# Kernel optimization log

Measured on AMD Instinct MI355X. Metric: run time of the kernel, lower is better.

## Reference

```python
import jax, jax.numpy as jnp
import numpy as np

B, S, HID, NH, DH = 2, 1024, 4096, 32, 128
ACT_BITS, W_BITS = 8, 4
NEG_INF = float(np.finfo(np.float32).min)


def _qdq(x, bits):
    """Symmetric fake-quant over the last axis (per-token / per-out-channel), with STE."""
    qmax = 2.0 ** (bits - 1) - 1
    s = jnp.maximum(jnp.max(jnp.abs(x), axis=-1, keepdims=True) / qmax, 1e-8)
    q = jnp.clip(jnp.round(x / s), -qmax - 1, qmax) * s
    return x + jax.lax.stop_gradient(q - x)


def _rope_tables(seq_len, dim):
    inv_freq = 1.0 / (10000.0 ** (np.arange(0, dim, 2, dtype=np.float32) / dim))
    t = np.arange(seq_len, dtype=np.float32)
    freqs = np.outer(t, inv_freq)              # [S, DH/2]
    emb = np.concatenate([freqs, freqs], -1)   # [S, DH]
    return jnp.asarray(np.cos(emb)), jnp.asarray(np.sin(emb))


def _rotate_half(x):
    h = x.shape[-1] // 2
    return jnp.concatenate([-x[..., h:], x[..., :h]], axis=-1)


def _norm(x):
    return jnp.linalg.norm(x, axis=-1, keepdims=True)


def setup_inputs() -> dict:
    key = jax.random.key(0)
    ks = jax.random.split(key, 5)
    causal = jnp.where(jnp.tril(jnp.ones((S, S), dtype=bool)), 0.0, NEG_INF).astype(jnp.float32)
    return {
        "hidden_states": jax.random.normal(ks[0], (B, S, HID), jnp.float32),
        "wq": jax.random.normal(ks[1], (HID, HID), jnp.float32) * 0.02,
        "wk": jax.random.normal(ks[2], (HID, HID), jnp.float32) * 0.02,
        "wv": jax.random.normal(ks[3], (HID, HID), jnp.float32) * 0.02,
        "wo": jax.random.normal(ks[4], (HID, HID), jnp.float32) * 0.02,
        "attention_mask": jnp.broadcast_to(causal[None, None], (B, 1, S, S)),
    }


def reference(hidden_states, wq, wk, wv, wo, attention_mask):
    cos, sin = _rope_tables(S, DH)
    cos, sin = cos[None, None], sin[None, None]          # [1,1,S,DH]
    x = _qdq(hidden_states, ACT_BITS)                    # act fake-quant (per token)

    def proj(w):
        return jnp.einsum('bsh,dh->bsd', x, _qdq(w, W_BITS)).reshape(B, S, NH, DH).transpose(0, 2, 1, 3)

    q, k, v = proj(wq), proj(wk), proj(wv)               # [B,H,S,D]
    q = q * cos + _rotate_half(q) * sin
    k = k * cos + _rotate_half(k) * sin

    # qkt_matmul: quant Q and K, rescale scores by quantization norm ratios a1, a2
    x1len = _norm(q)
    qq = _qdq(q, ACT_BITS)
    a1 = _norm(qq) / x1len                               # [B,H,S,1]
    x2len = _norm(k)
    kq = _qdq(k, ACT_BITS)
    a2 = jnp.swapaxes(_norm(kq) / x2len, 2, 3)           # [B,H,1,S]

    attn = jnp.einsum('bhqd,bhkd->bhqk', qq, kq) / np.float32(np.sqrt(DH))
    attn = attn / a1 / a2
    attn = attn + attention_mask
    attn = jnp.maximum(attn, NEG_INF)
    p = jax.nn.softmax(attn.astype(jnp.float32), axis=-1)

    # pv_matmul: quant P and V, rescale output by V's norm ratio
    pq = _qdq(p, ACT_BITS)
    x2len_v = _norm(v)
    vq = _qdq(v, ACT_BITS)
    a2v = _norm(vq) / x2len_v                            # [B,H,S,1]

    out = jnp.einsum('bhqk,bhkd->bhqd', pq, vq) / a2v    # [B,H,S,D]
    out = out.transpose(0, 2, 1, 3).reshape(B, S, HID)
    out = jnp.einsum('bsh,dh->bsd', _qdq(out, ACT_BITS), _qdq(wo, W_BITS))
    return out
```

## Files before the change

### kernel.cpp

```cpp
#include <hip/hip_runtime.h>
#include <hip/hip_bf16.h>
#include <math.h>
#include <stdint.h>

#define NEG_INF_F (-3.4028234663852886e38f)

typedef __bf16 bf16_t;
typedef __bf16 bf16x8 __attribute__((ext_vector_type(8)));
typedef float f32x4 __attribute__((ext_vector_type(4)));
typedef float f32x16 __attribute__((ext_vector_type(16)));
typedef int i32x4 __attribute__((ext_vector_type(4)));
typedef int i32x16 __attribute__((ext_vector_type(16)));
typedef int8_t c8x4 __attribute__((ext_vector_type(4)));

static constexpr int Bb = 2, Ss = 1024, Hid = 4096, Nh = 32, Dh = 128;
static constexpr int Mr = Bb * Ss;
static constexpr int Bh = Bb * Nh;

__device__ __forceinline__ void gload_lds16(const void* g, void* l) {
  __builtin_amdgcn_global_load_lds((const __attribute__((address_space(1))) void*)g,
                                   (__attribute__((address_space(3))) void*)l, 16, 0, 0);
}

__device__ __forceinline__ float wred_max(float v) {
#pragma unroll
  for (int off = 32; off > 0; off >>= 1) v = fmaxf(v, __shfl_xor(v, off));
  return v;
}

__device__ __forceinline__ unsigned pkbf(float a, float b) {
  unsigned short ua = __builtin_bit_cast(unsigned short, (bf16_t)a);
  unsigned short ub = __builtin_bit_cast(unsigned short, (bf16_t)b);
  return (unsigned)ua | ((unsigned)ub << 16);
}

__global__ void rope_table_kernel(float* __restrict__ ctab, float* __restrict__ stab) {
  int i = blockIdx.x * 256 + threadIdx.x;
  int srow = i >> 6, d = i & 63;
  float invf = (float)pow(10000.0, -((double)(2 * d) / (double)Dh));
  float ang = (float)srow * invf;
  ctab[i] = (float)cos((double)ang);
  stab[i] = (float)sin((double)ang);
}

__global__ __launch_bounds__(256) void quant_rows_kernel(
    const float* __restrict__ in, int8_t* __restrict__ outq,
    float* __restrict__ scale, int ncols, float qmax, float clo, float chi)
{
  const int row = blockIdx.x;
  const float* x = in + (size_t)row * ncols;
  int8_t* o = outq + (size_t)row * ncols;
  const int tid = threadIdx.x;
  const float4* x4 = (const float4*)x;
  const int n4 = ncols >> 2;
  float m = 0.f;
  for (int i = tid; i < n4; i += 256) {
    float4 v = x4[i];
    m = fmaxf(m, fmaxf(fmaxf(fabsf(v.x), fabsf(v.y)), fmaxf(fabsf(v.z), fabsf(v.w))));
  }
  m = wred_max(m);
  __shared__ float red[4];
  if ((tid & 63) == 0) red[tid >> 6] = m;
  __syncthreads();
  m = fmaxf(fmaxf(red[0], red[1]), fmaxf(red[2], red[3]));
  const float s = fmaxf(m / qmax, 1e-8f);
  if (tid == 0) scale[row] = s;
  c8x4* o4 = (c8x4*)o;
  for (int i = tid; i < n4; i += 256) {
    float4 v = x4[i];
    c8x4 r;
    r[0] = (int8_t)(int)fminf(fmaxf(rintf(v.x / s), clo), chi);
    r[1] = (int8_t)(int)fminf(fmaxf(rintf(v.y / s), clo), chi);
    r[2] = (int8_t)(int)fminf(fmaxf(rintf(v.z / s), clo), chi);
    r[3] = (int8_t)(int)fminf(fmaxf(rintf(v.w / s), clo), chi);
    o4[i] = r;
  }
}

template <int MODE>
__global__ __launch_bounds__(256) void gemm_kernel(
    const int8_t* __restrict__ A, const float* __restrict__ sA,
    const int8_t* __restrict__ W, const float* __restrict__ sW,
    float* __restrict__ out0,
    int8_t* __restrict__ outq, float* __restrict__ Ff,
    bf16_t* __restrict__ vdq, float* __restrict__ a2vp,
    const float* __restrict__ ctab, const float* __restrict__ stab,
    int M, int N, int K)
{
  __shared__ __align__(16) int8_t As[128 * 64];
  __shared__ __align__(16) int8_t Bs[128 * 64];
  __shared__ float s_red[2][128][3];
  __shared__ __align__(16) char smem_vt[MODE == 3 ? (128 * 136 * 2) : 16];

  const int tid = threadIdx.x, lane = tid & 63, wid = tid >> 6;
  const int id = blockIdx.x;
  const int xcd = id & 7, within = id >> 3;
  const int nIdx = xcd * 4 + (within >> 4);
  const int mIdx = within & 15;
  const int bm = mIdx * 128, bn = nIdx * 128;

  const int wm = wid >> 1, wn = wid & 1;
  const int l15 = lane & 15, kg = lane >> 4;
  const int ckey = (l15 >> 1) & 3;

  const int srowL = wid * 16 + (lane >> 2);
  const int skin = ((lane & 3) ^ ((lane >> 3) & 3)) * 16;
  const int8_t* gA = A + (size_t)(bm + srowL) * K + skin;
  const int8_t* gB = W + (size_t)(bn + srowL) * K + skin;
  const size_t half = (size_t)64 * K;
  int8_t* lA = As + wid * 1024;
  int8_t* lB = Bs + wid * 1024;

  i32x4 acc[4][4] = {};
  for (int k0 = 0; k0 < K; k0 += 64) {
    if (k0) __syncthreads();
    gload_lds16(gA + k0, lA);
    gload_lds16(gA + k0 + half, lA + 4096);
    gload_lds16(gB + k0, lB);
    gload_lds16(gB + k0 + half, lB + 4096);
    __syncthreads();
    i32x4 af[4], bw[4];
#pragma unroll
    for (int f = 0; f < 4; ++f) {
      af[f] = *(const i32x4*)&As[(wm * 64 + f * 16 + l15) * 64 + (kg ^ ckey) * 16];
      bw[f] = *(const i32x4*)&Bs[(f * 32 + wn * 16 + l15) * 64 + (kg ^ ckey) * 16];
    }
#pragma unroll
    for (int fm = 0; fm < 4; ++fm)
#pragma unroll
      for (int fn = 0; fn < 4; ++fn)
        acc[fm][fn] = __builtin_amdgcn_mfma_i32_16x16x64_i8(af[fm], bw[fn], acc[fm][fn], 0, 0, 0);
  }

  float sav[4][4], swv[4];
#pragma unroll
  for (int fm = 0; fm < 4; ++fm)
#pragma unroll
    for (int j = 0; j < 4; ++j) sav[fm][j] = sA[bm + wm * 64 + fm * 16 + kg * 4 + j];
#pragma unroll
  for (int fn = 0; fn < 4; ++fn) swv[fn] = sW[bn + fn * 32 + wn * 16 + l15];

  float val[4][4][4];
#pragma unroll
  for (int fm = 0; fm < 4; ++fm)
#pragma unroll
    for (int fn = 0; fn < 4; ++fn)
#pragma unroll
      for (int j = 0; j < 4; ++j)
        val[fm][fn][j] = (float)acc[fm][fn][j] * sav[fm][j] * swv[fn];

  if constexpr (MODE == 0) {
#pragma unroll
    for (int fm = 0; fm < 4; ++fm)
#pragma unroll
      for (int j = 0; j < 4; ++j) {
        const int row = bm + wm * 64 + fm * 16 + kg * 4 + j;
#pragma unroll
        for (int fn = 0; fn < 4; ++fn)
          out0[(size_t)row * N + bn + fn * 32 + wn * 16 + l15] = val[fm][fn][j];
      }
  } else {
    const int b = bm >> 10;
    const int bh = b * Nh + nIdx;
    float r_[4][4][4];
    if constexpr (MODE == 2) {
      const int dmA = wn * 16 + l15, dmB = 32 + wn * 16 + l15;
#pragma unroll
      for (int fm = 0; fm < 4; ++fm)
#pragma unroll
        for (int j = 0; j < 4; ++j) {
          const int srow = (bm + wm * 64 + fm * 16 + kg * 4 + j) & (Ss - 1);
          const float cA = ctab[srow * 64 + dmA], cB = ctab[srow * 64 + dmB];
          const float sA_ = stab[srow * 64 + dmA], sB_ = stab[srow * 64 + dmB];
          r_[fm][0][j] = __fsub_rn(__fmul_rn(val[fm][0][j], cA), __fmul_rn(val[fm][2][j], sA_));
          r_[fm][1][j] = __fsub_rn(__fmul_rn(val[fm][1][j], cB), __fmul_rn(val[fm][3][j], sB_));
          r_[fm][2][j] = __fadd_rn(__fmul_rn(val[fm][2][j], cA), __fmul_rn(val[fm][0][j], sA_));
          r_[fm][3][j] = __fadd_rn(__fmul_rn(val[fm][3][j], cB), __fmul_rn(val[fm][1][j], sB_));
        }
    } else {
#pragma unroll
      for (int fm = 0; fm < 4; ++fm)
#pragma unroll
        for (int fn = 0; fn < 4; ++fn)
#pragma unroll
          for (int j = 0; j < 4; ++j) r_[fm][fn][j] = val[fm][fn][j];
    }
    float ma_[4][4], n2_[4][4];
#pragma unroll
    for (int fm = 0; fm < 4; ++fm)
#pragma unroll
      for (int j = 0; j < 4; ++j) {
        float ma = 0.f, n2 = 0.f;
#pragma unroll
        for (int fn = 0; fn < 4; ++fn) {
          const float x = r_[fm][fn][j];
          ma = fmaxf(ma, fabsf(x));
          n2 += x * x;
        }
#pragma unroll
        for (int off = 1; off < 16; off <<= 1) {
          ma = fmaxf(ma, __shfl_xor(ma, off));
          n2 += __shfl_xor(n2, off);
        }
        ma_[fm][j] = ma;
        n2_[fm][j] = n2;
      }
    if (l15 == 0) {
#pragma unroll
      for (int fm = 0; fm < 4; ++fm)
#pragma unroll
        for (int j = 0; j < 4; ++j) {
          const int rl = wm * 64 + fm * 16 + kg * 4 + j;
          s_red[wn][rl][0] = ma_[fm][j];
          s_red[wn][rl][1] = n2_[fm][j];
        }
    }
    __syncthreads();
    float qc[4][4][4], svl[4][4], n2c[4][4], nq2_[4][4];
#pragma unroll
    for (int fm = 0; fm < 4; ++fm)
#pragma unroll
      for (int j = 0; j < 4; ++j) {
        const int rl = wm * 64 + fm * 16 + kg * 4 + j;
        const float ma = fmaxf(ma_[fm][j], s_red[wn ^ 1][rl][0]);
        const float n2 = n2_[fm][j] + s_red[wn ^ 1][rl][1];
        const float s = fmaxf(ma / 127.0f, 1e-8f);
        float nq2 = 0.f;
#pragma unroll
        for (int fn = 0; fn < 4; ++fn) {
          const float q = fminf(fmaxf(rintf(r_[fm][fn][j] / s), -128.f), 127.f);
          qc[fm][fn][j] = q;
          nq2 += q * q;
        }
#pragma unroll
        for (int off = 1; off < 16; off <<= 1) nq2 += __shfl_xor(nq2, off);
        svl[fm][j] = s;
        n2c[fm][j] = n2;
        nq2_[fm][j] = nq2;
      }
    if (l15 == 0) {
#pragma unroll
      for (int fm = 0; fm < 4; ++fm)
#pragma unroll
        for (int j = 0; j < 4; ++j)
          s_red[wn][wm * 64 + fm * 16 + kg * 4 + j][2] = nq2_[fm][j];
    }
    __syncthreads();

    if constexpr (MODE == 2) {
#pragma unroll
      for (int fm = 0; fm < 4; ++fm)
#pragma unroll
        for (int j = 0; j < 4; ++j) {
          const int rl = wm * 64 + fm * 16 + kg * 4 + j;
          const int stok = (bm + rl) & (Ss - 1);
          const size_t rowBase = ((size_t)bh * Ss + stok) * Dh;
#pragma unroll
          for (int fn = 0; fn < 4; ++fn)
            outq[rowBase + fn * 32 + wn * 16 + l15] = (int8_t)(int)qc[fm][fn][j];
          if (wn == 0 && l15 == 0) {
            const float nq2 = nq2_[fm][j] + s_red[1][rl][2];
            Ff[(size_t)bh * Ss + stok] = sqrtf(n2c[fm][j] / nq2) * 0.2973017787506803f;
          }
        }
    } else {
      bf16_t* svt = (bf16_t*)smem_vt;
#pragma unroll
      for (int fm = 0; fm < 4; ++fm)
#pragma unroll
        for (int j = 0; j < 4; ++j) {
          const int t = wm * 64 + fm * 16 + kg * 4 + j;
#pragma unroll
          for (int fn = 0; fn < 4; ++fn) {
            const int d = fn * 32 + wn * 16 + l15;
            svt[d * 136 + t] = (bf16_t)(qc[fm][fn][j] * svl[fm][j]);
          }
          if (wn == 0 && l15 == 0) {
            const float nq2 = nq2_[fm][j] + s_red[1][t][2];
            a2vp[(size_t)bh * Ss + ((bm + t) & (Ss - 1))] =
                svl[fm][j] * sqrtf(nq2) / sqrtf(n2c[fm][j]);
          }
        }
      __syncthreads();
      const int d = tid >> 1, toff = (tid & 1) * 64;
      const int s0 = bm & (Ss - 1);
      const bf16_t* src = svt + d * 136 + toff;
      bf16_t* dst = vdq + ((size_t)bh * Dh + d) * Ss + s0 + toff;
#pragma unroll
      for (int k = 0; k < 8; ++k) {
        bf16x8 tv;
#pragma unroll
        for (int e = 0; e < 8; ++e) tv[e] = src[k * 8 + e];
        *(bf16x8*)(dst + k * 8) = tv;
      }
    }
  }
}

#define KR(r) (((r) & 3) + 8 * ((r) >> 2) + 4 * hi)
__global__ __launch_bounds__(64, 2) void attn_kernel(
    const int8_t* __restrict__ qq, const int8_t* __restrict__ kq,
    const bf16_t* __restrict__ vdqt,
    const float* __restrict__ Fq, const float* __restrict__ Fk,
    const float* __restrict__ A2v, float* __restrict__ oattn)
{
  const int bh = blockIdx.x, b = bh >> 5, h = bh & 31;
  const int lane = threadIdx.x & 63;
  const int l31 = lane & 31, hi = lane >> 5;
  const int u = 31 - (int)blockIdx.y;
  const int q0 = u * 32;
  const int nt = u + 1;
  const size_t bhS = (size_t)bh * Ss;

  const int8_t* qrow = qq + (bhS + q0 + l31) * Dh + hi * 16;
  i32x4 qf[4];
#pragma unroll
  for (int c = 0; c < 4; ++c) qf[c] = *(const i32x4*)(qrow + c * 32);
  const float fq = Fq[bhS + q0 + l31];
  const int qcol = q0 + l31;

  float m = NEG_INF_F;
  int t = 0;
  for (; t + 1 < nt; t += 2) {
    const int kb0 = t * 32, kb1 = kb0 + 32;
    const int8_t* kr0 = kq + (bhS + kb0 + l31) * Dh + hi * 16;
    const int8_t* kr1 = kq + (bhS + kb1 + l31) * Dh + hi * 16;
    i32x16 ca = {}, cb = {}, da = {}, db = {};
    ca = __builtin_amdgcn_mfma_i32_32x32x32_i8(*(const i32x4*)(kr0),      qf[0], ca, 0, 0, 0);
    cb = __builtin_amdgcn_mfma_i32_32x32x32_i8(*(const i32x4*)(kr0 + 64), qf[2], cb, 0, 0, 0);
    da = __builtin_amdgcn_mfma_i32_32x32x32_i8(*(const i32x4*)(kr1),      qf[0], da, 0, 0, 0);
    db = __builtin_amdgcn_mfma_i32_32x32x32_i8(*(const i32x4*)(kr1 + 64), qf[2], db, 0, 0, 0);
    ca = __builtin_amdgcn_mfma_i32_32x32x32_i8(*(const i32x4*)(kr0 + 32), qf[1], ca, 0, 0, 0);
    cb = __builtin_amdgcn_mfma_i32_32x32x32_i8(*(const i32x4*)(kr0 + 96), qf[3], cb, 0, 0, 0);
    da = __builtin_amdgcn_mfma_i32_32x32x32_i8(*(const i32x4*)(kr1 + 32), qf[1], da, 0, 0, 0);
    db = __builtin_amdgcn_mfma_i32_32x32x32_i8(*(const i32x4*)(kr1 + 96), qf[3], db, 0, 0, 0);
    float4 fk40[4], fk41[4];
#pragma unroll
    for (int g = 0; g < 4; ++g) fk40[g] = *(const float4*)&Fk[bhS + kb0 + g * 8 + 4 * hi];
#pragma unroll
    for (int g = 0; g < 4; ++g) fk41[g] = *(const float4*)&Fk[bhS + kb1 + g * 8 + 4 * hi];
    const bool diag1 = (t + 1 == nt - 1);
#pragma unroll
    for (int r = 0; r < 16; ++r) {
      m = fmaxf(m, (float)(ca[r] + cb[r]) * fq * ((const float*)&fk40[r >> 2])[r & 3]);
      const float v1 = (float)(da[r] + db[r]) * fq * ((const float*)&fk41[r >> 2])[r & 3];
      if (!diag1 || (kb1 + KR(r) <= qcol)) m = fmaxf(m, v1);
    }
  }
  if (t < nt) {
    const int kb = t * 32;
    const int8_t* krow = kq + (bhS + kb + l31) * Dh + hi * 16;
    i32x16 ca = {}, cb = {};
    ca = __builtin_amdgcn_mfma_i32_32x32x32_i8(*(const i32x4*)(krow),      qf[0], ca, 0, 0, 0);
    cb = __builtin_amdgcn_mfma_i32_32x32x32_i8(*(const i32x4*)(krow + 64), qf[2], cb, 0, 0, 0);
    ca = __builtin_amdgcn_mfma_i32_32x32x32_i8(*(const i32x4*)(krow + 32), qf[1], ca, 0, 0, 0);
    cb = __builtin_amdgcn_mfma_i32_32x32x32_i8(*(const i32x4*)(krow + 96), qf[3], cb, 0, 0, 0);
    float4 fk4[4];
#pragma unroll
    for (int g = 0; g < 4; ++g) fk4[g] = *(const float4*)&Fk[bhS + kb + g * 8 + 4 * hi];
#pragma unroll
    for (int r = 0; r < 16; ++r) {
      const float v = (float)(ca[r] + cb[r]) * fq * ((const float*)&fk4[r >> 2])[r & 3];
      if (kb + KR(r) <= qcol) m = fmaxf(m, v);
    }
  }
  m = fmaxf(m, __shfl_xor(m, 32));

  float z = 0.f;
  f32x16 oacc[4] = {};
  for (int tt = 0; tt < nt; ++tt) {
    const int kb = tt * 32;
    const int8_t* krow = kq + (bhS + kb + l31) * Dh + hi * 16;
    i32x16 ca = {}, cb = {};
    ca = __builtin_amdgcn_mfma_i32_32x32x32_i8(*(const i32x4*)(krow),      qf[0], ca, 0, 0, 0);
    cb = __builtin_amdgcn_mfma_i32_32x32x32_i8(*(const i32x4*)(krow + 64), qf[2], cb, 0, 0, 0);
    ca = __builtin_amdgcn_mfma_i32_32x32x32_i8(*(const i32x4*)(krow + 32), qf[1], ca, 0, 0, 0);
    cb = __builtin_amdgcn_mfma_i32_32x32x32_i8(*(const i32x4*)(krow + 96), qf[3], cb, 0, 0, 0);
    float4 fk4[4];
#pragma unroll
    for (int g = 0; g < 4; ++g) fk4[g] = *(const float4*)&Fk[bhS + kb + g * 8 + 4 * hi];
    float p[16];
    const bool diag = (tt == nt - 1);
#pragma unroll
    for (int r = 0; r < 16; ++r) {
      float v = (float)(ca[r] + cb[r]) * fq * ((const float*)&fk4[r >> 2])[r & 3];
      if (diag && (kb + KR(r) > qcol)) v = NEG_INF_F;
      const float e = __expf(v - m);
      z += e;
      p[r] = rintf(127.0f * e);
    }
#pragma unroll
    for (int s = 0; s < 2; ++s) {
      const int rs = s * 8;
      unsigned k0 = pkbf(p[rs + 0], p[rs + 1]);
      unsigned k1 = pkbf(p[rs + 2], p[rs + 3]);
      unsigned k2 = pkbf(p[rs + 4], p[rs + 5]);
      unsigned k3 = pkbf(p[rs + 6], p[rs + 7]);
      unsigned sx0 = __shfl_xor(k0, 32);
      unsigned sx1 = __shfl_xor(k1, 32);
      unsigned sx2 = __shfl_xor(k2, 32);
      unsigned sx3 = __shfl_xor(k3, 32);
      uint4 ww;
      ww.x = hi ? sx2 : k0;
      ww.y = hi ? sx3 : k1;
      ww.z = hi ? k2 : sx0;
      ww.w = hi ? k3 : sx1;
      const bf16x8 af = __builtin_bit_cast(bf16x8, ww);
      const int kg2 = kb + s * 16 + hi * 8;
#pragma unroll
      for (int dt = 0; dt < 4; ++dt) {
        const bf16x8 vf = *(const bf16x8*)(vdqt + ((size_t)bh * Dh + dt * 32 + l31) * Ss + kg2);
        oacc[dt] = __builtin_amdgcn_mfma_f32_32x32x16_bf16(af, vf, oacc[dt], 0, 0, 0);
      }
    }
  }
  z += __shfl_xor(z, 32);
  const float osc = (1.0f / z) / 127.0f / A2v[bhS + q0 + l31];
#pragma unroll
  for (int dt = 0; dt < 4; ++dt) {
#pragma unroll
    for (int r = 0; r < 16; ++r) {
      const int q = q0 + KR(r);
      const float oscr = __shfl(osc, KR(r));
      oattn[((size_t)b * Ss + q) * Hid + h * Dh + dt * 32 + l31] = oacc[dt][r] * oscr;
    }
  }
}

extern "C" void kernel_launch(void* const* d_in, const int* in_sizes, int n_in,
                              void* d_out, int out_size, void* d_ws, size_t ws_size,
                              hipStream_t stream)
{
  const float* hidden = (const float*)d_in[0];
  const float* wq = (const float*)d_in[1];
  const float* wk = (const float*)d_in[2];
  const float* wv = (const float*)d_in[3];
  const float* wo = (const float*)d_in[4];
  float* out = (float*)d_out;

  char* p = (char*)d_ws;
  auto alloc = [&](size_t bytes) -> char* {
    char* r = p; p += (bytes + 255) & ~(size_t)255; return r;
  };
  int8_t* xq   = (int8_t*)alloc((size_t)Mr * Hid);
  int8_t* wbuf = (int8_t*)alloc((size_t)Hid * Hid);
  float*  oat  = (float*) alloc((size_t)Bh * Ss * Dh * sizeof(float));
  int8_t* qqb  = (int8_t*)alloc((size_t)Bh * Ss * Dh);
  int8_t* kqb  = (int8_t*)alloc((size_t)Bh * Ss * Dh);
  bf16_t* vdqt = (bf16_t*)alloc((size_t)Bh * Dh * Ss * sizeof(bf16_t));
  float* sxa = (float*)alloc((size_t)Mr * sizeof(float));
  float* sw  = (float*)alloc((size_t)Hid * sizeof(float));
  float* Fq  = (float*)alloc((size_t)Bh * Ss * sizeof(float));
  float* Fk  = (float*)alloc((size_t)Bh * Ss * sizeof(float));
  float* A2v = (float*)alloc((size_t)Bh * Ss * sizeof(float));
  float* soa = (float*)alloc((size_t)Mr * sizeof(float));
  float* ctab = (float*)alloc((size_t)Ss * 64 * sizeof(float));
  float* stab = (float*)alloc((size_t)Ss * 64 * sizeof(float));
  int8_t* oq  = xq;

  rope_table_kernel<<<Ss * 64 / 256, 256, 0, stream>>>(ctab, stab);
  quant_rows_kernel<<<Mr, 256, 0, stream>>>(hidden, xq, sxa, Hid, 127.f, -128.f, 127.f);

  quant_rows_kernel<<<Hid, 256, 0, stream>>>(wq, wbuf, sw, Hid, 7.f, -8.f, 7.f);
  gemm_kernel<2><<<512, 256, 0, stream>>>(xq, sxa, wbuf, sw, nullptr, qqb, Fq,
                                          nullptr, nullptr, ctab, stab, Mr, Hid, Hid);
  quant_rows_kernel<<<Hid, 256, 0, stream>>>(wk, wbuf, sw, Hid, 7.f, -8.f, 7.f);
  gemm_kernel<2><<<512, 256, 0, stream>>>(xq, sxa, wbuf, sw, nullptr, kqb, Fk,
                                          nullptr, nullptr, ctab, stab, Mr, Hid, Hid);
  quant_rows_kernel<<<Hid, 256, 0, stream>>>(wv, wbuf, sw, Hid, 7.f, -8.f, 7.f);
  gemm_kernel<3><<<512, 256, 0, stream>>>(xq, sxa, wbuf, sw, nullptr, nullptr, nullptr,
                                          vdqt, A2v, ctab, stab, Mr, Hid, Hid);

  dim3 ga(Bh, 32);
  attn_kernel<<<ga, 64, 0, stream>>>(qqb, kqb, vdqt, Fq, Fk, A2v, oat);

  quant_rows_kernel<<<Mr, 256, 0, stream>>>(oat, oq, soa, Hid, 127.f, -128.f, 127.f);
  quant_rows_kernel<<<Hid, 256, 0, stream>>>(wo, wbuf, sw, Hid, 7.f, -8.f, 7.f);
  gemm_kernel<0><<<512, 256, 0, stream>>>(oq, soa, wbuf, sw, out, nullptr, nullptr,
                                          nullptr, nullptr, nullptr, nullptr, Mr, Hid, Hid);
}
```

Baseline: 411.2 us.

## Fuse QKV weight quant and GEMMs into single launches with 128-deep K tiles

Quantizes wq/wk/wv in one batched kernel into separate buffers and runs one QKV GEMM grid of 1536 blocks that picks the weight and epilogue (RoPE+quant for Q/K, transposed dequant for V) per block. The K step doubles to 128 with a new 8-chunk XOR swizzle, halving barrier iterations in both the QKV and output GEMMs. The goal is fewer launches, better GPU fill from a larger grid, and less sync overhead. In exchange it needs three weight buffers and more LDS per block, which may lower occupancy.

```diff
diff --git a/kernel.cpp b/kernel.cpp
--- a/kernel.cpp
+++ b/kernel.cpp
@@ -43,13 +43,10 @@
   stab[i] = (float)sin((double)ang);
 }
 
-__global__ __launch_bounds__(256) void quant_rows_kernel(
-    const float* __restrict__ in, int8_t* __restrict__ outq,
-    float* __restrict__ scale, int ncols, float qmax, float clo, float chi)
-{
-  const int row = blockIdx.x;
-  const float* x = in + (size_t)row * ncols;
-  int8_t* o = outq + (size_t)row * ncols;
+__device__ __forceinline__ void quant_row_body(
+    const float* __restrict__ x, int8_t* __restrict__ o, float* __restrict__ scale,
+    int row, int ncols, float qmax, float clo, float chi)
+{
   const int tid = threadIdx.x;
   const float4* x4 = (const float4*)x;
   const int n4 = ncols >> 2;
@@ -77,221 +74,299 @@
   }
 }
 
-template <int MODE>
-__global__ __launch_bounds__(256) void gemm_kernel(
+__global__ __launch_bounds__(256) void quant_rows_kernel(
+    const float* __restrict__ in, int8_t* __restrict__ outq,
+    float* __restrict__ scale, int ncols, float qmax, float clo, float chi)
+{
+  const int row = blockIdx.x;
+  quant_row_body(in + (size_t)row * ncols, outq + (size_t)row * ncols, scale,
+                 row, ncols, qmax, clo, chi);
+}
+
+__global__ __launch_bounds__(256) void quant_w3_kernel(
+    const float* __restrict__ w0, const float* __restrict__ w1, const float* __restrict__ w2,
+    int8_t* __restrict__ o0, int8_t* __restrict__ o1, int8_t* __restrict__ o2,
+    float* __restrict__ s0, float* __restrict__ s1, float* __restrict__ s2)
+{
+  const int sel = blockIdx.x >> 12, row = blockIdx.x & 4095;
+  const float* in = sel == 0 ? w0 : (sel == 1 ? w1 : w2);
+  int8_t* o = sel == 0 ? o0 : (sel == 1 ? o1 : o2);
+  float* sc = sel == 0 ? s0 : (sel == 1 ? s1 : s2);
+  quant_row_body(in + (size_t)row * Hid, o + (size_t)row * Hid, sc, row, Hid,
+                 7.f, -8.f, 7.f);
+}
+
+__global__ __launch_bounds__(256) void qkv_gemm_kernel(
+    const int8_t* __restrict__ A, const float* __restrict__ sA,
+    const int8_t* __restrict__ wqz, const int8_t* __restrict__ wkz, const int8_t* __restrict__ wvz,
+    const float* __restrict__ swq, const float* __restrict__ swk, const float* __restrict__ swv,
+    int8_t* __restrict__ qqb, float* __restrict__ Fq,
+    int8_t* __restrict__ kqb, float* __restrict__ Fk,
+    bf16_t* __restrict__ vdq, float* __restrict__ a2vp,
+    const float* __restrict__ ctab, const float* __restrict__ stab)
+{
+  __shared__ __align__(16) char smem[34816 + 3072];
+  int8_t* As = (int8_t*)smem;
+  int8_t* Bs = (int8_t*)(smem + 16384);
+  float (*s_red)[128][3] = (float (*)[128][3])(smem + 34816);
+
+  const int tid = threadIdx.x, lane = tid & 63, wid = tid >> 6;
+  const int id = blockIdx.x;
+  const int xcd = id & 7, within = id >> 3;
+  const int nIdx = xcd * 12 + (within >> 4);
+  const int mIdx = within & 15;
+  const int wsel = nIdx >> 5, head = nIdx & 31;
+  const int bm = mIdx * 128, bn = head * 128;
+  const int8_t* W = wsel == 0 ? wqz : (wsel == 1 ? wkz : wvz);
+  const float* sW = wsel == 0 ? swq : (wsel == 1 ? swk : swv);
+  constexpr int K = Hid;
+
+  const int wm = wid >> 1, wn = wid & 1;
+  const int l15 = lane & 15, kg4 = lane >> 4;
+
+  const int strow = wid * 8 + (lane >> 3);
+  const int schunk = ((lane & 7) ^ (lane >> 3)) * 16;
+  const int8_t* gA = A + (size_t)(bm + strow) * K + schunk;
+  const int8_t* gB = W + (size_t)(bn + strow) * K + schunk;
+
+  i32x4 acc[4][4] = {};
+  for (int k0 = 0; k0 < K; k0 += 128) {
+    if (k0) __syncthreads();
+#pragma unroll
+    for (int r = 0; r < 4; ++r) {
+      gload_lds16(gA + k0 + (size_t)r * 32 * K, As + r * 4096 + wid * 1024);
+      gload_lds16(gB + k0 + (size_t)r * 32 * K, Bs + r * 4096 + wid * 1024);
+    }
+    __syncthreads();
+#pragma unroll
+    for (int g = 0; g < 2; ++g) {
+      i32x4 af[4], bw[4];
+#pragma unroll
+      for (int f = 0; f < 4; ++f) {
+        const int ca = (((g << 2) | kg4) ^ (l15 & 7)) * 16;
+        af[f] = *(const i32x4*)&As[(wm * 64 + f * 16 + l15) * 128 + ca];
+        bw[f] = *(const i32x4*)&Bs[(f * 32 + wn * 16 + l15) * 128 + ca];
+      }
+#pragma unroll
+      for (int fm = 0; fm < 4; ++fm)
+#pragma unroll
+        for (int fn = 0; fn < 4; ++fn)
+          acc[fm][fn] = __builtin_amdgcn_mfma_i32_16x16x64_i8(af[fm], bw[fn], acc[fm][fn], 0, 0, 0);
+    }
+  }
+
+  float sav[4][4], swv_[4];
+#pragma unroll
+  for (int fm = 0; fm < 4; ++fm)
+#pragma unroll
+    for (int j = 0; j < 4; ++j) sav[fm][j] = sA[bm + wm * 64 + fm * 16 + kg4 * 4 + j];
+#pragma unroll
+  for (int fn = 0; fn < 4; ++fn) swv_[fn] = sW[bn + fn * 32 + wn * 16 + l15];
+
+  float val[4][4][4];
+#pragma unroll
+  for (int fm = 0; fm < 4; ++fm)
+#pragma unroll
+    for (int fn = 0; fn < 4; ++fn)
+#pragma unroll
+      for (int j = 0; j < 4; ++j)
+        val[fm][fn][j] = (float)acc[fm][fn][j] * sav[fm][j] * swv_[fn];
+
+  const int b = bm >> 10;
+  const int bh = b * Nh + head;
+  float r_[4][4][4];
+  if (wsel != 2) {
+    const int dmA = wn * 16 + l15, dmB = 32 + wn * 16 + l15;
+#pragma unroll
+    for (int fm = 0; fm < 4; ++fm)
+#pragma unroll
+      for (int j = 0; j < 4; ++j) {
+        const int srow = (bm + wm * 64 + fm * 16 + kg4 * 4 + j) & (Ss - 1);
+        const float cA = ctab[srow * 64 + dmA], cB = ctab[srow * 64 + dmB];
+        const float sA_ = stab[srow * 64 + dmA], sB_ = stab[srow * 64 + dmB];
+        r_[fm][0][j] = __fsub_rn(__fmul_rn(val[fm][0][j], cA), __fmul_rn(val[fm][2][j], sA_));
+        r_[fm][1][j] = __fsub_rn(__fmul_rn(val[fm][1][j], cB), __fmul_rn(val[fm][3][j], sB_));
+        r_[fm][2][j] = __fadd_rn(__fmul_rn(val[fm][2][j], cA), __fmul_rn(val[fm][0][j], sA_));
+        r_[fm][3][j] = __fadd_rn(__fmul_rn(val[fm][3][j], cB), __fmul_rn(val[fm][1][j], sB_));
+      }
+  } else {
+#pragma unroll
+    for (int fm = 0; fm < 4; ++fm)
+#pragma unroll
+      for (int fn = 0; fn < 4; ++fn)
+#pragma unroll
+        for (int j = 0; j < 4; ++j) r_[fm][fn][j] = val[fm][fn][j];
+  }
+  float ma_[4][4], n2_[4][4];
+#pragma unroll
+  for (int fm = 0; fm < 4; ++fm)
+#pragma unroll
+    for (int j = 0; j < 4; ++j) {
+      float ma = 0.f, n2 = 0.f;
+#pragma unroll
+      for (int fn = 0; fn < 4; ++fn) {
+        const float x = r_[fm][fn][j];
+        ma = fmaxf(ma, fabsf(x));
+        n2 += x * x;
+      }
+#pragma unroll
+      for (int off = 1; off < 16; off <<= 1) {
+        ma = fmaxf(ma, __shfl_xor(ma, off));
+        n2 += __shfl_xor(n2, off);
+      }
+      ma_[fm][j] = ma;
+      n2_[fm][j] = n2;
+    }
+  if (l15 == 0) {
+#pragma unroll
+    for (int fm = 0; fm < 4; ++fm)
+#pragma unroll
+      for (int j = 0; j < 4; ++j) {
+        const int rl = wm * 64 + fm * 16 + kg4 * 4 + j;
+        s_red[wn][rl][0] = ma_[fm][j];
+        s_red[wn][rl][1] = n2_[fm][j];
+      }
+  }
+  __syncthreads();
+  float qc[4][4][4], svl[4][4], n2c[4][4], nq2_[4][4];
+#pragma unroll
+  for (int fm = 0; fm < 4; ++fm)
+#pragma unroll
+    for (int j = 0; j < 4; ++j) {
+      const int rl = wm * 64 + fm * 16 + kg4 * 4 + j;
+      const float ma = fmaxf(ma_[fm][j], s_red[wn ^ 1][rl][0]);
+      const float n2 = n2_[fm][j] + s_red[wn ^ 1][rl][1];
+      const float s = fmaxf(ma / 127.0f, 1e-8f);
+      float nq2 = 0.f;
+#pragma unroll
+      for (int fn = 0; fn < 4; ++fn) {
+        const float q = fminf(fmaxf(rintf(r_[fm][fn][j] / s), -128.f), 127.f);
+        qc[fm][fn][j] = q;
+        nq2 += q * q;
+      }
+#pragma unroll
+      for (int off = 1; off < 16; off <<= 1) nq2 += __shfl_xor(nq2, off);
+      svl[fm][j] = s;
+      n2c[fm][j] = n2;
+      nq2_[fm][j] = nq2;
+    }
+  __syncthreads();
+  if (l15 == 0) {
+#pragma unroll
+    for (int fm = 0; fm < 4; ++fm)
+#pragma unroll
+      for (int j = 0; j < 4; ++j)
+        s_red[wn][wm * 64 + fm * 16 + kg4 * 4 + j][2] = nq2_[fm][j];
+  }
+  __syncthreads();
+
+  if (wsel != 2) {
+    int8_t* outq = (wsel == 0) ? qqb : kqb;
+    float* Ff = (wsel == 0) ? Fq : Fk;
+#pragma unroll
+    for (int fm = 0; fm < 4; ++fm)
+#pragma unroll
+      for (int j = 0; j < 4; ++j) {
+        const int rl = wm * 64 + fm * 16 + kg4 * 4 + j;
+        const int stok = (bm + rl) & (Ss - 1);
+        const size_t rowBase = ((size_t)bh * Ss + stok) * Dh;
+#pragma unroll
+        for (int fn = 0; fn < 4; ++fn)
+          outq[rowBase + fn * 32 + wn * 16 + l15] = (int8_t)(int)qc[fm][fn][j];
+        if (wn == 0 && l15 == 0) {
+          const float nq2 = nq2_[fm][j] + s_red[1][rl][2];
+          Ff[(size_t)bh * Ss + stok] = sqrtf(n2c[fm][j] / nq2) * 0.2973017787506803f;
+        }
+      }
+  } else {
+    bf16_t* svt = (bf16_t*)smem;
+#pragma unroll
+    for (int fm = 0; fm < 4; ++fm)
+#pragma unroll
+      for (int j = 0; j < 4; ++j) {
+        const int t = wm * 64 + fm * 16 + kg4 * 4 + j;
+#pragma unroll
+        for (int fn = 0; fn < 4; ++fn) {
+          const int d = fn * 32 + wn * 16 + l15;
+          svt[d * 136 + t] = (bf16_t)(qc[fm][fn][j] * svl[fm][j]);
+        }
+        if (wn == 0 && l15 == 0) {
+          const float nq2 = nq2_[fm][j] + s_red[1][t][2];
+          a2vp[(size_t)bh * Ss + ((bm + t) & (Ss - 1))] =
+              svl[fm][j] * sqrtf(nq2) / sqrtf(n2c[fm][j]);
+        }
+      }
+    __syncthreads();
+    const int d = tid >> 1, toff = (tid & 1) * 64;
+    const int s0 = bm & (Ss - 1);
+    const bf16_t* src = svt + d * 136 + toff;
+    bf16_t* dst = vdq + ((size_t)bh * Dh + d) * Ss + s0 + toff;
+#pragma unroll
+    for (int k = 0; k < 8; ++k) {
+      bf16x8 tv;
+#pragma unroll
+      for (int e = 0; e < 8; ++e) tv[e] = src[k * 8 + e];
+      *(bf16x8*)(dst + k * 8) = tv;
+    }
+  }
+}
+
+__global__ __launch_bounds__(256) void gemm0_kernel(
     const int8_t* __restrict__ A, const float* __restrict__ sA,
     const int8_t* __restrict__ W, const float* __restrict__ sW,
-    float* __restrict__ out0,
-    int8_t* __restrict__ outq, float* __restrict__ Ff,
-    bf16_t* __restrict__ vdq, float* __restrict__ a2vp,
-    const float* __restrict__ ctab, const float* __restrict__ stab,
-    int M, int N, int K)
-{
-  __shared__ __align__(16) int8_t As[128 * 64];
-  __shared__ __align__(16) int8_t Bs[128 * 64];
-  __shared__ float s_red[2][128][3];
-  __shared__ __align__(16) char smem_vt[MODE == 3 ? (128 * 136 * 2) : 16];
-
+    float* __restrict__ out, int M, int N, int K)
+{
+  __shared__ __align__(16) int8_t As[128 * 128];
+  __shared__ __align__(16) int8_t Bs[128 * 128];
   const int tid = threadIdx.x, lane = tid & 63, wid = tid >> 6;
   const int id = blockIdx.x;
   const int xcd = id & 7, within = id >> 3;
   const int nIdx = xcd * 4 + (within >> 4);
   const int mIdx = within & 15;
   const int bm = mIdx * 128, bn = nIdx * 128;
-
   const int wm = wid >> 1, wn = wid & 1;
-  const int l15 = lane & 15, kg = lane >> 4;
-  const int ckey = (l15 >> 1) & 3;
-
-  const int srowL = wid * 16 + (lane >> 2);
-  const int skin = ((lane & 3) ^ ((lane >> 3) & 3)) * 16;
-  const int8_t* gA = A + (size_t)(bm + srowL) * K + skin;
-  const int8_t* gB = W + (size_t)(bn + srowL) * K + skin;
-  const size_t half = (size_t)64 * K;
-  int8_t* lA = As + wid * 1024;
-  int8_t* lB = Bs + wid * 1024;
+  const int l15 = lane & 15, kg4 = lane >> 4;
+
+  const int strow = wid * 8 + (lane >> 3);
+  const int schunk = ((lane & 7) ^ (lane >> 3)) * 16;
+  const int8_t* gA = A + (size_t)(bm + strow) * K + schunk;
+  const int8_t* gB = W + (size_t)(bn + strow) * K + schunk;
 
   i32x4 acc[4][4] = {};
-  for (int k0 = 0; k0 < K; k0 += 64) {
+  for (int k0 = 0; k0 < K; k0 += 128) {
     if (k0) __syncthreads();
-    gload_lds16(gA + k0, lA);
-    gload_lds16(gA + k0 + half, lA + 4096);
-    gload_lds16(gB + k0, lB);
-    gload_lds16(gB + k0 + half, lB + 4096);
+#pragma unroll
+    for (int r = 0; r < 4; ++r) {
+      gload_lds16(gA + k0 + (size_t)r * 32 * K, As + r * 4096 + wid * 1024);
+      gload_lds16(gB + k0 + (size_t)r * 32 * K, Bs + r * 4096 + wid * 1024);
+    }
     __syncthreads();
-    i32x4 af[4], bw[4];
-#pragma unroll
-    for (int f = 0; f < 4; ++f) {
-      af[f] = *(const i32x4*)&As[(wm * 64 + f * 16 + l15) * 64 + (kg ^ ckey) * 16];
-      bw[f] = *(const i32x4*)&Bs[(f * 32 + wn * 16 + l15) * 64 + (kg ^ ckey) * 16];
-    }
-#pragma unroll
-    for (int fm = 0; fm < 4; ++fm)
-#pragma unroll
-      for (int fn = 0; fn < 4; ++fn)
-        acc[fm][fn] = __builtin_amdgcn_mfma_i32_16x16x64_i8(af[fm], bw[fn], acc[fm][fn], 0, 0, 0);
-  }
-
-  float sav[4][4], swv[4];
-#pragma unroll
-  for (int fm = 0; fm < 4; ++fm)
-#pragma unroll
-    for (int j = 0; j < 4; ++j) sav[fm][j] = sA[bm + wm * 64 + fm * 16 + kg * 4 + j];
-#pragma unroll
-  for (int fn = 0; fn < 4; ++fn) swv[fn] = sW[bn + fn * 32 + wn * 16 + l15];
-
-  float val[4][4][4];
-#pragma unroll
-  for (int fm = 0; fm < 4; ++fm)
-#pragma unroll
-    for (int fn = 0; fn < 4; ++fn)
-#pragma unroll
-      for (int j = 0; j < 4; ++j)
-        val[fm][fn][j] = (float)acc[fm][fn][j] * sav[fm][j] * swv[fn];
-
-  if constexpr (MODE == 0) {
-#pragma unroll
-    for (int fm = 0; fm < 4; ++fm)
-#pragma unroll
-      for (int j = 0; j < 4; ++j) {
-        const int row = bm + wm * 64 + fm * 16 + kg * 4 + j;
+#pragma unroll
+    for (int g = 0; g < 2; ++g) {
+      i32x4 af[4], bw[4];
+#pragma unroll
+      for (int f = 0; f < 4; ++f) {
+        const int ca = (((g << 2) | kg4) ^ (l15 & 7)) * 16;
+        af[f] = *(const i32x4*)&As[(wm * 64 + f * 16 + l15) * 128 + ca];
+        bw[f] = *(const i32x4*)&Bs[(f * 32 + wn * 16 + l15) * 128 + ca];
+      }
+#pragma unroll
+      for (int fm = 0; fm < 4; ++fm)
 #pragma unroll
         for (int fn = 0; fn < 4; ++fn)
-          out0[(size_t)row * N + bn + fn * 32 + wn * 16 + l15] = val[fm][fn][j];
-      }
-  } else {
-    const int b = bm >> 10;
-    const int bh = b * Nh + nIdx;
-    float r_[4][4][4];
-    if constexpr (MODE == 2) {
-      const int dmA = wn * 16 + l15, dmB = 32 + wn * 16 + l15;
-#pragma unroll
-      for (int fm = 0; fm < 4; ++fm)
-#pragma unroll
-        for (int j = 0; j < 4; ++j) {
-          const int srow = (bm + wm * 64 + fm * 16 + kg * 4 + j) & (Ss - 1);
-          const float cA = ctab[srow * 64 + dmA], cB = ctab[srow * 64 + dmB];
-          const float sA_ = stab[srow * 64 + dmA], sB_ = stab[srow * 64 + dmB];
-          r_[fm][0][j] = __fsub_rn(__fmul_rn(val[fm][0][j], cA), __fmul_rn(val[fm][2][j], sA_));
-          r_[fm][1][j] = __fsub_rn(__fmul_rn(val[fm][1][j], cB), __fmul_rn(val[fm][3][j], sB_));
-          r_[fm][2][j] = __fadd_rn(__fmul_rn(val[fm][2][j], cA), __fmul_rn(val[fm][0][j], sA_));
-          r_[fm][3][j] = __fadd_rn(__fmul_rn(val[fm][3][j], cB), __fmul_rn(val[fm][1][j], sB_));
-        }
-    } else {
-#pragma unroll
-      for (int fm = 0; fm < 4; ++fm)
-#pragma unroll
-        for (int fn = 0; fn < 4; ++fn)
-#pragma unroll
-          for (int j = 0; j < 4; ++j) r_[fm][fn][j] = val[fm][fn][j];
-    }
-    float ma_[4][4], n2_[4][4];
-#pragma unroll
-    for (int fm = 0; fm < 4; ++fm)
-#pragma unroll
-      for (int j = 0; j < 4; ++j) {
-        float ma = 0.f, n2 = 0.f;
-#pragma unroll
-        for (int fn = 0; fn < 4; ++fn) {
-          const float x = r_[fm][fn][j];
-          ma = fmaxf(ma, fabsf(x));
-          n2 += x * x;
-        }
-#pragma unroll
-        for (int off = 1; off < 16; off <<= 1) {
-          ma = fmaxf(ma, __shfl_xor(ma, off));
-          n2 += __shfl_xor(n2, off);
-        }
-        ma_[fm][j] = ma;
-        n2_[fm][j] = n2;
-      }
-    if (l15 == 0) {
-#pragma unroll
-      for (int fm = 0; fm < 4; ++fm)
-#pragma unroll
-        for (int j = 0; j < 4; ++j) {
-          const int rl = wm * 64 + fm * 16 + kg * 4 + j;
-          s_red[wn][rl][0] = ma_[fm][j];
-          s_red[wn][rl][1] = n2_[fm][j];
-        }
-    }
-    __syncthreads();
-    float qc[4][4][4], svl[4][4], n2c[4][4], nq2_[4][4];
-#pragma unroll
-    for (int fm = 0; fm < 4; ++fm)
-#pragma unroll
-      for (int j = 0; j < 4; ++j) {
-        const int rl = wm * 64 + fm * 16 + kg * 4 + j;
-        const float ma = fmaxf(ma_[fm][j], s_red[wn ^ 1][rl][0]);
-        const float n2 = n2_[fm][j] + s_red[wn ^ 1][rl][1];
-        const float s = fmaxf(ma / 127.0f, 1e-8f);
-        float nq2 = 0.f;
-#pragma unroll
-        for (int fn = 0; fn < 4; ++fn) {
-          const float q = fminf(fmaxf(rintf(r_[fm][fn][j] / s), -128.f), 127.f);
-          qc[fm][fn][j] = q;
-          nq2 += q * q;
-        }
-#pragma unroll
-        for (int off = 1; off < 16; off <<= 1) nq2 += __shfl_xor(nq2, off);
-        svl[fm][j] = s;
-        n2c[fm][j] = n2;
-        nq2_[fm][j] = nq2;
-      }
-    if (l15 == 0) {
-#pragma unroll
-      for (int fm = 0; fm < 4; ++fm)
-#pragma unroll
-        for (int j = 0; j < 4; ++j)
-          s_red[wn][wm * 64 + fm * 16 + kg * 4 + j][2] = nq2_[fm][j];
-    }
-    __syncthreads();
-
-    if constexpr (MODE == 2) {
-#pragma unroll
-      for (int fm = 0; fm < 4; ++fm)
-#pragma unroll
-        for (int j = 0; j < 4; ++j) {
-          const int rl = wm * 64 + fm * 16 + kg * 4 + j;
-          const int stok = (bm + rl) & (Ss - 1);
-          const size_t rowBase = ((size_t)bh * Ss + stok) * Dh;
-#pragma unroll
-          for (int fn = 0; fn < 4; ++fn)
-            outq[rowBase + fn * 32 + wn * 16 + l15] = (int8_t)(int)qc[fm][fn][j];
-          if (wn == 0 && l15 == 0) {
-            const float nq2 = nq2_[fm][j] + s_red[1][rl][2];
-            Ff[(size_t)bh * Ss + stok] = sqrtf(n2c[fm][j] / nq2) * 0.2973017787506803f;
-          }
-        }
-    } else {
-      bf16_t* svt = (bf16_t*)smem_vt;
-#pragma unroll
-      for (int fm = 0; fm < 4; ++fm)
-#pragma unroll
-        for (int j = 0; j < 4; ++j) {
-          const int t = wm * 64 + fm * 16 + kg * 4 + j;
-#pragma unroll
-          for (int fn = 0; fn < 4; ++fn) {
-            const int d = fn * 32 + wn * 16 + l15;
-            svt[d * 136 + t] = (bf16_t)(qc[fm][fn][j] * svl[fm][j]);
-          }
-          if (wn == 0 && l15 == 0) {
-            const float nq2 = nq2_[fm][j] + s_red[1][t][2];
-            a2vp[(size_t)bh * Ss + ((bm + t) & (Ss - 1))] =
-                svl[fm][j] * sqrtf(nq2) / sqrtf(n2c[fm][j]);
-          }
-        }
-      __syncthreads();
-      const int d = tid >> 1, toff = (tid & 1) * 64;
-      const int s0 = bm & (Ss - 1);
-      const bf16_t* src = svt + d * 136 + toff;
-      bf16_t* dst = vdq + ((size_t)bh * Dh + d) * Ss + s0 + toff;
-#pragma unroll
-      for (int k = 0; k < 8; ++k) {
-        bf16x8 tv;
-#pragma unroll
-        for (int e = 0; e < 8; ++e) tv[e] = src[k * 8 + e];
-        *(bf16x8*)(dst + k * 8) = tv;
+          acc[fm][fn] = __builtin_amdgcn_mfma_i32_16x16x64_i8(af[fm], bw[fn], acc[fm][fn], 0, 0, 0);
+    }
+  }
+#pragma unroll
+  for (int fm = 0; fm < 4; ++fm) {
+#pragma unroll
+    for (int j = 0; j < 4; ++j) {
+      const int row = bm + wm * 64 + fm * 16 + kg4 * 4 + j;
+      const float sa = sA[row];
+#pragma unroll
+      for (int fn = 0; fn < 4; ++fn) {
+        const int col = bn + fn * 32 + wn * 16 + l15;
+        out[(size_t)row * N + col] = (float)acc[fm][fn][j] * sa * sW[col];
       }
     }
   }
@@ -443,13 +518,17 @@
     char* r = p; p += (bytes + 255) & ~(size_t)255; return r;
   };
   int8_t* xq   = (int8_t*)alloc((size_t)Mr * Hid);
-  int8_t* wbuf = (int8_t*)alloc((size_t)Hid * Hid);
+  int8_t* wb0  = (int8_t*)alloc((size_t)Hid * Hid);
+  int8_t* wb1  = (int8_t*)alloc((size_t)Hid * Hid);
+  int8_t* wb2  = (int8_t*)alloc((size_t)Hid * Hid);
   float*  oat  = (float*) alloc((size_t)Bh * Ss * Dh * sizeof(float));
   int8_t* qqb  = (int8_t*)alloc((size_t)Bh * Ss * Dh);
   int8_t* kqb  = (int8_t*)alloc((size_t)Bh * Ss * Dh);
   bf16_t* vdqt = (bf16_t*)alloc((size_t)Bh * Dh * Ss * sizeof(bf16_t));
   float* sxa = (float*)alloc((size_t)Mr * sizeof(float));
-  float* sw  = (float*)alloc((size_t)Hid * sizeof(float));
+  float* sw0 = (float*)alloc((size_t)Hid * sizeof(float));
+  float* sw1 = (float*)alloc((size_t)Hid * sizeof(float));
+  float* sw2 = (float*)alloc((size_t)Hid * sizeof(float));
   float* Fq  = (float*)alloc((size_t)Bh * Ss * sizeof(float));
   float* Fk  = (float*)alloc((size_t)Bh * Ss * sizeof(float));
   float* A2v = (float*)alloc((size_t)Bh * Ss * sizeof(float));
@@ -460,22 +539,15 @@
 
   rope_table_kernel<<<Ss * 64 / 256, 256, 0, stream>>>(ctab, stab);
   quant_rows_kernel<<<Mr, 256, 0, stream>>>(hidden, xq, sxa, Hid, 127.f, -128.f, 127.f);
-
-  quant_rows_kernel<<<Hid, 256, 0, stream>>>(wq, wbuf, sw, Hid, 7.f, -8.f, 7.f);
-  gemm_kernel<2><<<512, 256, 0, stream>>>(xq, sxa, wbuf, sw, nullptr, qqb, Fq,
-                                          nullptr, nullptr, ctab, stab, Mr, Hid, Hid);
-  quant_rows_kernel<<<Hid, 256, 0, stream>>>(wk, wbuf, sw, Hid, 7.f, -8.f, 7.f);
-  gemm_kernel<2><<<512, 256, 0, stream>>>(xq, sxa, wbuf, sw, nullptr, kqb, Fk,
-                                          nullptr, nullptr, ctab, stab, Mr, Hid, Hid);
-  quant_rows_kernel<<<Hid, 256, 0, stream>>>(wv, wbuf, sw, Hid, 7.f, -8.f, 7.f);
-  gemm_kernel<3><<<512, 256, 0, stream>>>(xq, sxa, wbuf, sw, nullptr, nullptr, nullptr,
-                                          vdqt, A2v, ctab, stab, Mr, Hid, Hid);
+  quant_w3_kernel<<<3 * Hid, 256, 0, stream>>>(wq, wk, wv, wb0, wb1, wb2, sw0, sw1, sw2);
+
+  qkv_gemm_kernel<<<1536, 256, 0, stream>>>(xq, sxa, wb0, wb1, wb2, sw0, sw1, sw2,
+                                            qqb, Fq, kqb, Fk, vdqt, A2v, ctab, stab);
 
   dim3 ga(Bh, 32);
   attn_kernel<<<ga, 64, 0, stream>>>(qqb, kqb, vdqt, Fq, Fk, A2v, oat);
 
   quant_rows_kernel<<<Mr, 256, 0, stream>>>(oat, oq, soa, Hid, 127.f, -128.f, 127.f);
-  quant_rows_kernel<<<Hid, 256, 0, stream>>>(wo, wbuf, sw, Hid, 7.f, -8.f, 7.f);
-  gemm_kernel<0><<<512, 256, 0, stream>>>(oq, soa, wbuf, sw, out, nullptr, nullptr,
-                                          nullptr, nullptr, nullptr, nullptr, Mr, Hid, Hid);
-}
+  quant_rows_kernel<<<Hid, 256, 0, stream>>>(wo, wb0, sw0, Hid, 7.f, -8.f, 7.f);
+  gemm0_kernel<<<512, 256, 0, stream>>>(oq, soa, wb0, sw0, out, Mr, Hid, Hid);
+}
```

After: 366.2 us (median of 2 runs). 1.12x faster.
